# Kernel optimization log

Measured on AMD Instinct MI355X. Metric: run time of the kernel, lower is better.

Reference implementation:

```python
import jax, jax.numpy as jnp
from jax import lax
import numpy as np

RADIUS = 0.2
NSAMPLE = 64


def setup_inputs() -> dict:
    key = jax.random.key(0)
    k1, k2, k3 = jax.random.split(key, 3)
    B, N, S, C = 4, 16384, 4096, 64
    xyz = jax.random.uniform(k1, (B, N, 3), dtype=jnp.float32)
    new_xyz = jax.random.uniform(k2, (B, S, 3), dtype=jnp.float32)
    features = jax.random.normal(k3, (B, C, N), dtype=jnp.float32)
    return {"xyz": xyz, "new_xyz": new_xyz, "features": features}


def _ball_query(xyz, new_xyz, radius, nsample):
    # xyz: (B,N,3), new_xyz: (B,S,3) -> idx (B,S,nsample) int32
    # Squared distances via GEMM form: ||q||^2 + ||p||^2 - 2 q.p
    N = xyz.shape[1]
    q2 = jnp.sum(new_xyz * new_xyz, axis=-1)            # (B,S)
    p2 = jnp.sum(xyz * xyz, axis=-1)                    # (B,N)
    qp = jnp.einsum('bsd,bnd->bsn', new_xyz, xyz)       # (B,S,N)
    d2 = q2[:, :, None] + p2[:, None, :] - 2.0 * qp     # (B,S,N)
    # CUDA ball_query semantics: take the FIRST nsample points (by index order)
    # within radius; pad remaining slots with the first found index; 0 if none.
    cand = jnp.where(d2 < radius * radius,
                     jnp.arange(N, dtype=jnp.int32), jnp.int32(N))  # (B,S,N)
    neg_smallest, _ = lax.top_k(-cand, nsample)         # nsample smallest indices
    idx = -neg_smallest                                 # ascending (B,S,nsample)
    first = idx[..., :1]
    idx = jnp.where(idx == N, first, idx)               # pad with first neighbor
    idx = jnp.where(idx == N, 0, idx)                   # no neighbor at all -> 0
    return idx


def _group(feat, idx):
    # feat: (B,C,N), idx: (B,S,K) -> (B,C,S,K)
    return jax.vmap(lambda f, i: f[:, i])(feat, idx)


def reference(xyz, new_xyz, features):
    idx = _ball_query(xyz, new_xyz, RADIUS, NSAMPLE)        # (B,S,K)
    grouped_xyz = _group(jnp.transpose(xyz, (0, 2, 1)), idx)  # (B,3,S,K)
    grouped_xyz = grouped_xyz - jnp.transpose(new_xyz, (0, 2, 1))[..., None]
    grouped_features = _group(features, idx)                # (B,C,S,K)
    return jnp.concatenate([grouped_xyz, grouped_features], axis=1)  # (B,3+C,S,K)
```

## Files before the change

kernel.cpp:

```cpp
#include <hip/hip_runtime.h>
#include <cstdint>
#include <cstddef>

#define BB 4
#define NN 16384
#define SS 4096
#define CC 64
#define NSAMP 64
#define R2 0.04f

typedef float f32x4 __attribute__((ext_vector_type(4)));

__global__ __launch_bounds__(256) void transpose_feat(const float* __restrict__ f,
                                                      float* __restrict__ ft) {
    __shared__ float tile[64][65];
    int blk = blockIdx.x;
    int b   = blk / (NN / 64);
    int n0  = (blk % (NN / 64)) * 64;
    int t   = threadIdx.x;
    int nl  = t & 63;
    int cq  = t >> 6;
#pragma unroll
    for (int p = 0; p < 16; ++p) {
        int c = cq + p * 4;
        tile[c][nl] = f[((size_t)b * CC + c) * NN + n0 + nl];
    }
    __syncthreads();
#pragma unroll
    for (int p = 0; p < 16; ++p) {
        int nl2 = cq + p * 4;
        ft[((size_t)b * NN + n0 + nl2) * CC + nl] = tile[nl][nl2];
    }
}

__global__ __launch_bounds__(256) void fused_qg(const float* __restrict__ xyz,
                                                const float* __restrict__ nxyz,
                                                const float* __restrict__ featT,
                                                float* __restrict__ out) {
    __shared__ float tile[64][65];
    __shared__ int   sidx[4][NSAMP];

    int t    = threadIdx.x;
    int wid  = t >> 6;
    int lane = t & 63;
    int wg   = blockIdx.x;
    int qblk = (wg & 7) * (BB * SS / 8 / 4) + (wg >> 3);
    int q0   = qblk * 4;

    {
        int q = q0 + wid;
        int b = q >> 12;
        int s = q & (SS - 1);
        const float* xb = xyz + (size_t)b * NN * 3;
        float qx = nxyz[((size_t)b * SS + s) * 3 + 0];
        float qy = nxyz[((size_t)b * SS + s) * 3 + 1];
        float qz = nxyz[((size_t)b * SS + s) * 3 + 2];
        float q2 = __fadd_rn(__fadd_rn(__fmul_rn(qx, qx), __fmul_rn(qy, qy)),
                             __fmul_rn(qz, qz));

        int cnt = 0;
        float px0 = xb[lane * 3 + 0], py0 = xb[lane * 3 + 1], pz0 = xb[lane * 3 + 2];
        float px1 = xb[(lane + 64) * 3 + 0], py1 = xb[(lane + 64) * 3 + 1],
              pz1 = xb[(lane + 64) * 3 + 2];
        for (int base = 0; base < NN; base += 128) {
            float ax = px0, ay = py0, az = pz0;
            float bx = px1, by = py1, bz = pz1;
            int nb = base + 128;
            if (nb < NN) {
                px0 = xb[(nb + lane) * 3 + 0];
                py0 = xb[(nb + lane) * 3 + 1];
                pz0 = xb[(nb + lane) * 3 + 2];
                px1 = xb[(nb + 64 + lane) * 3 + 0];
                py1 = xb[(nb + 64 + lane) * 3 + 1];
                pz1 = xb[(nb + 64 + lane) * 3 + 2];
            }
            float p2a = __fadd_rn(__fadd_rn(__fmul_rn(ax, ax), __fmul_rn(ay, ay)),
                                  __fmul_rn(az, az));
            float qpa = __fadd_rn(__fadd_rn(__fmul_rn(qx, ax), __fmul_rn(qy, ay)),
                                  __fmul_rn(qz, az));
            float d2a = __fsub_rn(__fadd_rn(q2, p2a), __fadd_rn(qpa, qpa));
            float p2b = __fadd_rn(__fadd_rn(__fmul_rn(bx, bx), __fmul_rn(by, by)),
                                  __fmul_rn(bz, bz));
            float qpb = __fadd_rn(__fadd_rn(__fmul_rn(qx, bx), __fmul_rn(qy, by)),
                                  __fmul_rn(qz, bz));
            float d2b = __fsub_rn(__fadd_rn(q2, p2b), __fadd_rn(qpb, qpb));
            bool in0 = d2a < R2;
            bool in1 = d2b < R2;
            unsigned long long m0 = __ballot(in0);
            unsigned long long m1 = __ballot(in1);
            int c0 = __popcll(m0);
            if (in0) {
                int pos = cnt + __popcll(m0 & ((1ull << lane) - 1ull));
                if (pos < NSAMP) sidx[wid][pos] = base + lane;
            }
            if (in1) {
                int pos = cnt + c0 + __popcll(m1 & ((1ull << lane) - 1ull));
                if (pos < NSAMP) sidx[wid][pos] = base + 64 + lane;
            }
            cnt += c0 + __popcll(m1);
            if (cnt >= NSAMP) break;
        }
        asm volatile("s_waitcnt lgkmcnt(0)" ::: "memory");
        int total = cnt < NSAMP ? cnt : NSAMP;
        int myidx = (total == 0) ? 0 : ((lane < total) ? sidx[wid][lane] : sidx[wid][0]);
        asm volatile("s_waitcnt lgkmcnt(0)" ::: "memory");
        sidx[wid][lane] = myidx;
    }
    __syncthreads();

    int rsub = t >> 4;
    int cf4  = t & 15;
    int k4   = t & 15;
#pragma unroll
    for (int qi = 0; qi < 4; ++qi) {
        int q = q0 + qi;
        int b = q >> 12;
        int s = q & (SS - 1);
        const float* ftb = featT + (size_t)b * NN * CC;
#pragma unroll
        for (int j = 0; j < 4; ++j) {
            int row = j * 16 + rsub;
            int pr  = sidx[qi][row];
            const f32x4 v = *(const f32x4*)(ftb + (size_t)pr * CC + cf4 * 4);
            tile[row][cf4 * 4 + 0] = v.x;
            tile[row][cf4 * 4 + 1] = v.y;
            tile[row][cf4 * 4 + 2] = v.z;
            tile[row][cf4 * 4 + 3] = v.w;
        }
        size_t obase = ((size_t)b * 67) * SS * 64 + (size_t)s * 64;
        size_t chs   = (size_t)SS * 64;
        if (wid == qi) {
            int id = sidx[qi][lane];
            float qx = nxyz[((size_t)b * SS + s) * 3 + 0];
            float qy = nxyz[((size_t)b * SS + s) * 3 + 1];
            float qz = nxyz[((size_t)b * SS + s) * 3 + 2];
            const float* xb = xyz + (size_t)b * NN * 3;
            float gx = __fsub_rn(xb[(size_t)id * 3 + 0], qx);
            float gy = __fsub_rn(xb[(size_t)id * 3 + 1], qy);
            float gz = __fsub_rn(xb[(size_t)id * 3 + 2], qz);
            __builtin_nontemporal_store(gx, out + obase + 0 * chs + lane);
            __builtin_nontemporal_store(gy, out + obase + 1 * chs + lane);
            __builtin_nontemporal_store(gz, out + obase + 2 * chs + lane);
        }
        __syncthreads();
#pragma unroll
        for (int j = 0; j < 4; ++j) {
            int c = j * 16 + (t >> 4);
            f32x4 o;
            o.x = tile[k4 * 4 + 0][c];
            o.y = tile[k4 * 4 + 1][c];
            o.z = tile[k4 * 4 + 2][c];
            o.w = tile[k4 * 4 + 3][c];
            __builtin_nontemporal_store(o,
                (f32x4*)(out + obase + (size_t)(3 + c) * chs + k4 * 4));
        }
        __syncthreads();
    }
}

__global__ __launch_bounds__(64) void qg_fallback(const float* __restrict__ xyz,
                                                  const float* __restrict__ nxyz,
                                                  const float* __restrict__ feat,
                                                  float* __restrict__ out) {
    __shared__ int sidx[NSAMP];
    int q = blockIdx.x;
    int b = q >> 12, s = q & (SS - 1);
    int lane = threadIdx.x;
    const float* xb = xyz + (size_t)b * NN * 3;
    float qx = nxyz[((size_t)b * SS + s) * 3 + 0];
    float qy = nxyz[((size_t)b * SS + s) * 3 + 1];
    float qz = nxyz[((size_t)b * SS + s) * 3 + 2];
    float q2 = __fadd_rn(__fadd_rn(__fmul_rn(qx, qx), __fmul_rn(qy, qy)),
                         __fmul_rn(qz, qz));
    int cnt = 0;
    for (int base = 0; base < NN; base += 64) {
        float cx = xb[(size_t)(base + lane) * 3 + 0];
        float cy = xb[(size_t)(base + lane) * 3 + 1];
        float cz = xb[(size_t)(base + lane) * 3 + 2];
        float p2 = __fadd_rn(__fadd_rn(__fmul_rn(cx, cx), __fmul_rn(cy, cy)),
                             __fmul_rn(cz, cz));
        float qp = __fadd_rn(__fadd_rn(__fmul_rn(qx, cx), __fmul_rn(qy, cy)),
                             __fmul_rn(qz, cz));
        float d2 = __fsub_rn(__fadd_rn(q2, p2), __fadd_rn(qp, qp));
        bool in = d2 < R2;
        unsigned long long m = __ballot(in);
        if (in) {
            int pos = cnt + __popcll(m & ((1ull << lane) - 1ull));
            if (pos < NSAMP) sidx[pos] = base + lane;
        }
        cnt += __popcll(m);
        if (cnt >= NSAMP) break;
    }
    __syncthreads();
    int total = cnt < NSAMP ? cnt : NSAMP;
    int myidx = (total == 0) ? 0 : ((lane < total) ? sidx[lane] : sidx[0]);
    size_t obase = ((size_t)b * 67) * SS * 64 + (size_t)s * 64;
    size_t chs   = (size_t)SS * 64;
    out[obase + 0 * chs + lane] = __fsub_rn(xb[(size_t)myidx * 3 + 0], qx);
    out[obase + 1 * chs + lane] = __fsub_rn(xb[(size_t)myidx * 3 + 1], qy);
    out[obase + 2 * chs + lane] = __fsub_rn(xb[(size_t)myidx * 3 + 2], qz);
    const float* fb = feat + (size_t)b * CC * NN;
#pragma unroll 4
    for (int c = 0; c < CC; ++c)
        out[obase + (size_t)(3 + c) * chs + lane] = fb[(size_t)c * NN + myidx];
}

extern "C" void kernel_launch(void* const* d_in, const int* in_sizes, int n_in,
                              void* d_out, int out_size, void* d_ws, size_t ws_size,
                              hipStream_t stream) {
    const float* xyz  = (const float*)d_in[0];
    const float* nxyz = (const float*)d_in[1];
    const float* feat = (const float*)d_in[2];
    float* out = (float*)d_out;

    size_t needT = (size_t)BB * NN * CC * sizeof(float);
    if (ws_size >= needT) {
        float* featT = (float*)d_ws;
        transpose_feat<<<BB * (NN / 64), 256, 0, stream>>>(feat, featT);
        fused_qg<<<BB * SS / 4, 256, 0, stream>>>(xyz, nxyz, featT, out);
    } else {
        qg_fallback<<<BB * SS, 64, 0, stream>>>(xyz, nxyz, feat, out);
    }
}
```

Measured before the change: 89.57 us.

## Make gather/transpose per-wave with shuffled indices and software-pipelined feature loads

Each wave now gathers and transposes the features for its own query, using a private 16x67 LDS sub-tile per chunk, instead of all four waves cooperating on each query with block-wide barriers. Neighbor indices are broadcast with shuffles rather than read back from LDS, and the next chunk's feature loads are issued before the current chunk is transposed and stored. This removes the __syncthreads between waves so that the ball-query imbalance across waves stops stalling the whole block. In exchange it uses more registers for the prefetched vectors and issues smaller per-wave store bursts.

New measurement: 115.8 us. +29.3%, slower.

```diff
diff --git a/kernel.cpp b/kernel.cpp
--- a/kernel.cpp
+++ b/kernel.cpp
@@ -8,6 +8,7 @@
 #define CC 64
 #define NSAMP 64
 #define R2 0.04f
+#define PAD 67
 
 typedef float f32x4 __attribute__((ext_vector_type(4)));
 
@@ -37,7 +38,7 @@
                                                 const float* __restrict__ nxyz,
                                                 const float* __restrict__ featT,
                                                 float* __restrict__ out) {
-    __shared__ float tile[64][65];
+    __shared__ float sub[4][16][PAD];
     __shared__ int   sidx[4][NSAMP];
 
     int t    = threadIdx.x;
@@ -45,116 +46,122 @@
     int lane = t & 63;
     int wg   = blockIdx.x;
     int qblk = (wg & 7) * (BB * SS / 8 / 4) + (wg >> 3);
-    int q0   = qblk * 4;
+    int q    = qblk * 4 + wid;
+    int b    = q >> 12;
+    int s    = q & (SS - 1);
+
+    const float* xb = xyz + (size_t)b * NN * 3;
+    float qx = nxyz[((size_t)b * SS + s) * 3 + 0];
+    float qy = nxyz[((size_t)b * SS + s) * 3 + 1];
+    float qz = nxyz[((size_t)b * SS + s) * 3 + 2];
+    float q2 = __fadd_rn(__fadd_rn(__fmul_rn(qx, qx), __fmul_rn(qy, qy)),
+                         __fmul_rn(qz, qz));
+
+    int cnt = 0;
+    float px0 = xb[lane * 3 + 0], py0 = xb[lane * 3 + 1], pz0 = xb[lane * 3 + 2];
+    float px1 = xb[(lane + 64) * 3 + 0], py1 = xb[(lane + 64) * 3 + 1],
+          pz1 = xb[(lane + 64) * 3 + 2];
+    for (int base = 0; base < NN; base += 128) {
+        float ax = px0, ay = py0, az = pz0;
+        float bx = px1, by = py1, bz = pz1;
+        int nb = base + 128;
+        if (nb < NN) {
+            px0 = xb[(nb + lane) * 3 + 0];
+            py0 = xb[(nb + lane) * 3 + 1];
+            pz0 = xb[(nb + lane) * 3 + 2];
+            px1 = xb[(nb + 64 + lane) * 3 + 0];
+            py1 = xb[(nb + 64 + lane) * 3 + 1];
+            pz1 = xb[(nb + 64 + lane) * 3 + 2];
+        }
+        float p2a = __fadd_rn(__fadd_rn(__fmul_rn(ax, ax), __fmul_rn(ay, ay)),
+                              __fmul_rn(az, az));
+        float qpa = __fadd_rn(__fadd_rn(__fmul_rn(qx, ax), __fmul_rn(qy, ay)),
+                              __fmul_rn(qz, az));
+        float d2a = __fsub_rn(__fadd_rn(q2, p2a), __fadd_rn(qpa, qpa));
+        float p2b = __fadd_rn(__fadd_rn(__fmul_rn(bx, bx), __fmul_rn(by, by)),
+                              __fmul_rn(bz, bz));
+        float qpb = __fadd_rn(__fadd_rn(__fmul_rn(qx, bx), __fmul_rn(qy, by)),
+                              __fmul_rn(qz, bz));
+        float d2b = __fsub_rn(__fadd_rn(q2, p2b), __fadd_rn(qpb, qpb));
+        bool in0 = d2a < R2;
+        bool in1 = d2b < R2;
+        unsigned long long m0 = __ballot(in0);
+        unsigned long long m1 = __ballot(in1);
+        int c0 = __popcll(m0);
+        if (in0) {
+            int pos = cnt + __popcll(m0 & ((1ull << lane) - 1ull));
+            if (pos < NSAMP) sidx[wid][pos] = base + lane;
+        }
+        if (in1) {
+            int pos = cnt + c0 + __popcll(m1 & ((1ull << lane) - 1ull));
+            if (pos < NSAMP) sidx[wid][pos] = base + 64 + lane;
+        }
+        cnt += c0 + __popcll(m1);
+        if (cnt >= NSAMP) break;
+    }
+    asm volatile("s_waitcnt lgkmcnt(0)" ::: "memory");
+    int total = cnt < NSAMP ? cnt : NSAMP;
+    int myidx = (total == 0) ? 0 : ((lane < total) ? sidx[wid][lane] : sidx[wid][0]);
+
+    size_t obase = ((size_t)b * 67) * SS * 64 + (size_t)s * 64;
+    size_t chs   = (size_t)SS * 64;
 
     {
-        int q = q0 + wid;
-        int b = q >> 12;
-        int s = q & (SS - 1);
-        const float* xb = xyz + (size_t)b * NN * 3;
-        float qx = nxyz[((size_t)b * SS + s) * 3 + 0];
-        float qy = nxyz[((size_t)b * SS + s) * 3 + 1];
-        float qz = nxyz[((size_t)b * SS + s) * 3 + 2];
-        float q2 = __fadd_rn(__fadd_rn(__fmul_rn(qx, qx), __fmul_rn(qy, qy)),
-                             __fmul_rn(qz, qz));
-
-        int cnt = 0;
-        float px0 = xb[lane * 3 + 0], py0 = xb[lane * 3 + 1], pz0 = xb[lane * 3 + 2];
-        float px1 = xb[(lane + 64) * 3 + 0], py1 = xb[(lane + 64) * 3 + 1],
-              pz1 = xb[(lane + 64) * 3 + 2];
-        for (int base = 0; base < NN; base += 128) {
-            float ax = px0, ay = py0, az = pz0;
-            float bx = px1, by = py1, bz = pz1;
-            int nb = base + 128;
-            if (nb < NN) {
-                px0 = xb[(nb + lane) * 3 + 0];
-                py0 = xb[(nb + lane) * 3 + 1];
-                pz0 = xb[(nb + lane) * 3 + 2];
-                px1 = xb[(nb + 64 + lane) * 3 + 0];
-                py1 = xb[(nb + 64 + lane) * 3 + 1];
-                pz1 = xb[(nb + 64 + lane) * 3 + 2];
+        float gx = __fsub_rn(xb[(size_t)myidx * 3 + 0], qx);
+        float gy = __fsub_rn(xb[(size_t)myidx * 3 + 1], qy);
+        float gz = __fsub_rn(xb[(size_t)myidx * 3 + 2], qz);
+        __builtin_nontemporal_store(gx, out + obase + 0 * chs + lane);
+        __builtin_nontemporal_store(gy, out + obase + 1 * chs + lane);
+        __builtin_nontemporal_store(gz, out + obase + 2 * chs + lane);
+    }
+
+    const float* ftb = featT + (size_t)b * NN * CC;
+    int fc   = lane & 15;
+    int rsub = lane >> 4;
+    int csub = lane >> 2;
+    int s4   = lane & 3;
+
+    f32x4 v[4];
+#pragma unroll
+    for (int j = 0; j < 4; ++j) {
+        int row = j * 4 + rsub;
+        int pr  = __shfl(myidx, row);
+        v[j] = *(const f32x4*)(ftb + (size_t)pr * CC + fc * 4);
+    }
+#pragma unroll
+    for (int chunk = 0; chunk < 4; ++chunk) {
+        f32x4 w[4];
+        if (chunk < 3) {
+#pragma unroll
+            for (int j = 0; j < 4; ++j) {
+                int row = (chunk + 1) * 16 + j * 4 + rsub;
+                int pr  = __shfl(myidx, row);
+                w[j] = *(const f32x4*)(ftb + (size_t)pr * CC + fc * 4);
             }
-            float p2a = __fadd_rn(__fadd_rn(__fmul_rn(ax, ax), __fmul_rn(ay, ay)),
-                                  __fmul_rn(az, az));
-            float qpa = __fadd_rn(__fadd_rn(__fmul_rn(qx, ax), __fmul_rn(qy, ay)),
-                                  __fmul_rn(qz, az));
-            float d2a = __fsub_rn(__fadd_rn(q2, p2a), __fadd_rn(qpa, qpa));
-            float p2b = __fadd_rn(__fadd_rn(__fmul_rn(bx, bx), __fmul_rn(by, by)),
-                                  __fmul_rn(bz, bz));
-            float qpb = __fadd_rn(__fadd_rn(__fmul_rn(qx, bx), __fmul_rn(qy, by)),
-                                  __fmul_rn(qz, bz));
-            float d2b = __fsub_rn(__fadd_rn(q2, p2b), __fadd_rn(qpb, qpb));
-            bool in0 = d2a < R2;
-            bool in1 = d2b < R2;
-            unsigned long long m0 = __ballot(in0);
-            unsigned long long m1 = __ballot(in1);
-            int c0 = __popcll(m0);
-            if (in0) {
-                int pos = cnt + __popcll(m0 & ((1ull << lane) - 1ull));
-                if (pos < NSAMP) sidx[wid][pos] = base + lane;
-            }
-            if (in1) {
-                int pos = cnt + c0 + __popcll(m1 & ((1ull << lane) - 1ull));
-                if (pos < NSAMP) sidx[wid][pos] = base + 64 + lane;
-            }
-            cnt += c0 + __popcll(m1);
-            if (cnt >= NSAMP) break;
+        }
+#pragma unroll
+        for (int j = 0; j < 4; ++j) {
+            int r = j * 4 + rsub;
+            sub[wid][r][fc * 4 + 0] = v[j].x;
+            sub[wid][r][fc * 4 + 1] = v[j].y;
+            sub[wid][r][fc * 4 + 2] = v[j].z;
+            sub[wid][r][fc * 4 + 3] = v[j].w;
         }
         asm volatile("s_waitcnt lgkmcnt(0)" ::: "memory");
-        int total = cnt < NSAMP ? cnt : NSAMP;
-        int myidx = (total == 0) ? 0 : ((lane < total) ? sidx[wid][lane] : sidx[wid][0]);
+#pragma unroll
+        for (int j = 0; j < 4; ++j) {
+            int c = j * 16 + csub;
+            f32x4 o;
+            o.x = sub[wid][s4 * 4 + 0][c];
+            o.y = sub[wid][s4 * 4 + 1][c];
+            o.z = sub[wid][s4 * 4 + 2][c];
+            o.w = sub[wid][s4 * 4 + 3][c];
+            __builtin_nontemporal_store(o,
+                (f32x4*)(out + obase + (size_t)(3 + c) * chs + chunk * 16 + s4 * 4));
+        }
         asm volatile("s_waitcnt lgkmcnt(0)" ::: "memory");
-        sidx[wid][lane] = myidx;
-    }
-    __syncthreads();
-
-    int rsub = t >> 4;
-    int cf4  = t & 15;
-    int k4   = t & 15;
-#pragma unroll
-    for (int qi = 0; qi < 4; ++qi) {
-        int q = q0 + qi;
-        int b = q >> 12;
-        int s = q & (SS - 1);
-        const float* ftb = featT + (size_t)b * NN * CC;
-#pragma unroll
-        for (int j = 0; j < 4; ++j) {
-            int row = j * 16 + rsub;
-            int pr  = sidx[qi][row];
-            const f32x4 v = *(const f32x4*)(ftb + (size_t)pr * CC + cf4 * 4);
-            tile[row][cf4 * 4 + 0] = v.x;
-            tile[row][cf4 * 4 + 1] = v.y;
-            tile[row][cf4 * 4 + 2] = v.z;
-            tile[row][cf4 * 4 + 3] = v.w;
-        }
-        size_t obase = ((size_t)b * 67) * SS * 64 + (size_t)s * 64;
-        size_t chs   = (size_t)SS * 64;
-        if (wid == qi) {
-            int id = sidx[qi][lane];
-            float qx = nxyz[((size_t)b * SS + s) * 3 + 0];
-            float qy = nxyz[((size_t)b * SS + s) * 3 + 1];
-            float qz = nxyz[((size_t)b * SS + s) * 3 + 2];
-            const float* xb = xyz + (size_t)b * NN * 3;
-            float gx = __fsub_rn(xb[(size_t)id * 3 + 0], qx);
-            float gy = __fsub_rn(xb[(size_t)id * 3 + 1], qy);
-            float gz = __fsub_rn(xb[(size_t)id * 3 + 2], qz);
-            __builtin_nontemporal_store(gx, out + obase + 0 * chs + lane);
-            __builtin_nontemporal_store(gy, out + obase + 1 * chs + lane);
-            __builtin_nontemporal_store(gz, out + obase + 2 * chs + lane);
-        }
-        __syncthreads();
-#pragma unroll
-        for (int j = 0; j < 4; ++j) {
-            int c = j * 16 + (t >> 4);
-            f32x4 o;
-            o.x = tile[k4 * 4 + 0][c];
-            o.y = tile[k4 * 4 + 1][c];
-            o.z = tile[k4 * 4 + 2][c];
-            o.w = tile[k4 * 4 + 3][c];
-            __builtin_nontemporal_store(o,
-                (f32x4*)(out + obase + (size_t)(3 + c) * chs + k4 * 4));
-        }
-        __syncthreads();
+#pragma unroll
+        for (int j = 0; j < 4; ++j) v[j] = w[j];
     }
 }
 
```
